# Kernel optimization log

Hardware: AMD Instinct MI355X
Metric: run time of the kernel (lower is better)

## Reference

```python
import jax, jax.numpy as jnp
import numpy as np
import math

N_HEAD = 16

def _c(a):
    # stack real/imag -> complex64
    return jax.lax.complex(a[..., 0], a[..., 1])

def _rope_phasor(T, D, dtype=jnp.float32):
    inv_freq = 1.0 / (10000.0 ** (jnp.arange(D, dtype=dtype) / D))
    t = jnp.arange(T, dtype=dtype)
    freqs = jnp.outer(t, inv_freq)  # [T, D]
    return jax.lax.complex(jnp.cos(freqs), jnp.sin(freqs))

def setup_inputs() -> dict:
    key = jax.random.key(0)
    ks = jax.random.split(key, 9)
    B, T, C = 2, 1024, 1024
    s = 0.02
    return {
        "x":  jax.random.normal(ks[0], (B, T, C, 2), jnp.float32),
        "wq": jax.random.normal(ks[1], (C, C, 2), jnp.float32) * s,
        "bq": jax.random.normal(ks[2], (C, 2), jnp.float32) * s,
        "wk": jax.random.normal(ks[3], (C, C, 2), jnp.float32) * s,
        "bk": jax.random.normal(ks[4], (C, 2), jnp.float32) * s,
        "wv": jax.random.normal(ks[5], (C, C, 2), jnp.float32) * s,
        "bv": jax.random.normal(ks[6], (C, 2), jnp.float32) * s,
        "wo": jax.random.normal(ks[7], (C, C, 2), jnp.float32) * s,
        "bo": jax.random.normal(ks[8], (C, 2), jnp.float32) * s,
    }

def reference(x, wq, bq, wk, bk, wv, bv, wo, bo):
    B, T, C, _ = x.shape
    H = N_HEAD
    D = C // H
    xc = _c(x)
    # complex linear projections: y = x @ W^T + b
    q = xc @ _c(wq).T + _c(bq)
    k = xc @ _c(wk).T + _c(bk)
    v = xc @ _c(wv).T + _c(bv)
    # [B, T, C] -> [B, H, T, D]
    q = q.reshape(B, T, H, D).transpose(0, 2, 1, 3)
    k = k.reshape(B, T, H, D).transpose(0, 2, 1, 3)
    v = v.reshape(B, T, H, D).transpose(0, 2, 1, 3)
    # complex RoPE phasor multiply
    ph = _rope_phasor(T, D)[None, None]  # [1,1,T,D]
    q = q * ph
    k = k * ph
    # complex QK^H, scaled
    score = jnp.einsum('bhtd,bhsd->bhts', q, jnp.conj(k)) / math.sqrt(D)
    # softmax over magnitude, then real-valued complex weights
    attn = jax.nn.softmax(jnp.abs(score), axis=-1)
    attn_c = jax.lax.complex(attn, jnp.zeros_like(attn))
    out = jnp.einsum('bhts,bhsd->bhtd', attn_c, v)
    out = out.transpose(0, 2, 1, 3).reshape(B, T, C)
    out = out @ _c(wo).T + _c(bo)
    # return real/imag stacked for a real-valued harness
    return jnp.stack([out.real, out.imag], axis=-1)
```

## Files before the change

### kernel.cpp

```cpp
#include <hip/hip_runtime.h>
#include <math.h>

#define T_SEQ  1024
#define C_DIM  1024
#define NH_    16
#define H_DIM  64
#define SCL    (0.125f * 1.4426950408889634f)

typedef __bf16 bf16;
typedef __bf16 bf16x4 __attribute__((ext_vector_type(4)));
typedef __bf16 bf16x8 __attribute__((ext_vector_type(8)));
typedef float  f32x4  __attribute__((ext_vector_type(4)));

#define MFMA16(a, b, c) __builtin_amdgcn_mfma_f32_16x16x32_bf16(a, b, c, 0, 0, 0)

#define GLOAD_LDS16(g, l) __builtin_amdgcn_global_load_lds( \
    (const __attribute__((address_space(1))) void*)(g),     \
    (__attribute__((address_space(3))) void*)(l), 16, 0, 0)

__device__ __forceinline__ bf16x8 neg8(bf16x8 x) {
    union { bf16x8 v; unsigned int u[4]; } t;
    t.v = x;
    t.u[0] ^= 0x80008000u; t.u[1] ^= 0x80008000u;
    t.u[2] ^= 0x80008000u; t.u[3] ^= 0x80008000u;
    return t.v;
}

__device__ __forceinline__ bf16x8 frag_sw(const bf16* plane, int row, int chunk) {
    int c = chunk ^ (row & 7);
    return *(const bf16x8*)&plane[row * 64 + c * 8];
}
__device__ __forceinline__ bf16x8 frag_sw4b(const bf16* plane, int row, int chunk) {
    int c = chunk ^ ((row >> 1) & 3);
    return *(const bf16x8*)&plane[row * 32 + c * 8];
}

__global__ __launch_bounds__(256)
void split_all(const float* __restrict__ x,  const float* __restrict__ wq,
               const float* __restrict__ wk, const float* __restrict__ wv,
               const float* __restrict__ wo,
               bf16* Xr, bf16* Xi, bf16* Wqr, bf16* Wqi, bf16* Wkr, bf16* Wki,
               bf16* Wvr, bf16* Wvi, bf16* Wor, bf16* Woi,
               float* __restrict__ rope)
{
    int z = blockIdx.y;
    if (z == 5) {
        if (blockIdx.x >= 256) return;
        int idx = blockIdx.x * 256 + threadIdx.x;
        int tp = idx >> 6, d = idx & 63;
        float invf = exp2f((float)d * -0.2076205059304601f);
        float fr = (float)tp * invf;
        float sn, cs; sincosf(fr, &sn, &cs);
        *(float2*)&rope[(size_t)idx * 2] = make_float2(cs, sn);
        return;
    }
    if (z > 0 && blockIdx.x >= 512) return;
    const float* in; bf16 *pr, *pi;
    if      (z == 0) { in = x;  pr = Xr;  pi = Xi;  }
    else if (z == 1) { in = wq; pr = Wqr; pi = Wqi; }
    else if (z == 2) { in = wk; pr = Wkr; pi = Wki; }
    else if (z == 3) { in = wv; pr = Wvr; pi = Wvi; }
    else             { in = wo; pr = Wor; pi = Woi; }
    int idx = (blockIdx.x * 256 + threadIdx.x) * 8;
    bf16x8 r, im;
#pragma unroll
    for (int j = 0; j < 4; j++) {
        float4 v = *(const float4*)(in + (size_t)idx * 2 + j * 4);
        r[2*j]   = (bf16)v.x; im[2*j]   = (bf16)v.y;
        r[2*j+1] = (bf16)v.z; im[2*j+1] = (bf16)v.w;
    }
    *(bf16x8*)(pr + idx) = r;
    *(bf16x8*)(pi + idx) = im;
}

__global__ __launch_bounds__(512, 2)
void qkv_gemm(const bf16* __restrict__ Xr, const bf16* __restrict__ Xi,
              const bf16* __restrict__ Wqr, const bf16* __restrict__ Wqi,
              const bf16* __restrict__ Wkr, const bf16* __restrict__ Wki,
              const bf16* __restrict__ Wvr, const bf16* __restrict__ Wvi,
              const float* __restrict__ bq, const float* __restrict__ bk,
              const float* __restrict__ bv, const float* __restrict__ rope,
              bf16* Qr, bf16* Qi, bf16* Kr, bf16* Ki, bf16* Vr, bf16* Vi)
{
    __shared__ __attribute__((aligned(16))) bf16 smem[40960];
    const int t = threadIdx.x, lane = t & 63, wave = t >> 6;
    const int wm = (wave >> 1) * 32, wn = (wave & 1) * 32;
    const int lm = lane & 15, quad = lane >> 4;
    const int lr4 = lane >> 2, sc4 = ((lane & 3) ^ ((lane >> 3) & 3)) * 8;
    const int h = blockIdx.x, m0 = blockIdx.y * 128, n0 = h * 64;

    auto stage = [&](int k0, int bsel) {
        bf16* bb_ = smem + bsel * 20480;
#pragma unroll
        for (int j = 0; j < 5; j++) {
            int c = wave + 8 * j;
            const bf16* src; bf16* dst;
            if (c < 8)       {                 src = Xr  + (size_t)(m0 + c * 16 + lr4) * C_DIM + k0 + sc4; dst = bb_ + c * 512; }
            else if (c < 16) { int u = c - 8;  src = Xi  + (size_t)(m0 + u * 16 + lr4) * C_DIM + k0 + sc4; dst = bb_ + 4096  + u * 512; }
            else if (c < 20) { int u = c - 16; src = Wqr + (size_t)(n0 + u * 16 + lr4) * C_DIM + k0 + sc4; dst = bb_ + 8192  + u * 512; }
            else if (c < 24) { int u = c - 20; src = Wqi + (size_t)(n0 + u * 16 + lr4) * C_DIM + k0 + sc4; dst = bb_ + 10240 + u * 512; }
            else if (c < 28) { int u = c - 24; src = Wkr + (size_t)(n0 + u * 16 + lr4) * C_DIM + k0 + sc4; dst = bb_ + 12288 + u * 512; }
            else if (c < 32) { int u = c - 28; src = Wki + (size_t)(n0 + u * 16 + lr4) * C_DIM + k0 + sc4; dst = bb_ + 14336 + u * 512; }
            else if (c < 36) { int u = c - 32; src = Wvr + (size_t)(n0 + u * 16 + lr4) * C_DIM + k0 + sc4; dst = bb_ + 16384 + u * 512; }
            else             { int u = c - 36; src = Wvi + (size_t)(n0 + u * 16 + lr4) * C_DIM + k0 + sc4; dst = bb_ + 18432 + u * 512; }
            GLOAD_LDS16(src, dst);
        }
    };

    f32x4 accr[3][2][2], acci[3][2][2];
#pragma unroll
    for (int p = 0; p < 3; p++)
#pragma unroll
        for (int i = 0; i < 2; i++)
#pragma unroll
            for (int j = 0; j < 2; j++) { accr[p][i][j] = (f32x4)0.f; acci[p][i][j] = (f32x4)0.f; }

    stage(0, 0);
    for (int it = 0; it < 32; it++) {
        __syncthreads();
        if (it < 31) stage((it + 1) * 32, (it + 1) & 1);
        const bf16* buf = smem + (it & 1) * 20480;

        bf16x8 ar[2], ai_[2];
#pragma unroll
        for (int i = 0; i < 2; i++) {
            ar[i]  = frag_sw4b(buf,        wm + i * 16 + lm, quad);
            ai_[i] = frag_sw4b(buf + 4096, wm + i * 16 + lm, quad);
        }
#pragma unroll
        for (int p = 0; p < 3; p++) {
            const bf16* bp = buf + 8192 + p * 4096;
            bf16x8 br_[2], bi_[2], bn_[2];
#pragma unroll
            for (int j = 0; j < 2; j++) {
                br_[j] = frag_sw4b(bp,        wn + j * 16 + lm, quad);
                bi_[j] = frag_sw4b(bp + 2048, wn + j * 16 + lm, quad);
                bn_[j] = neg8(bi_[j]);
            }
#pragma unroll
            for (int i = 0; i < 2; i++)
#pragma unroll
                for (int j = 0; j < 2; j++) {
                    accr[p][i][j] = MFMA16(ar[i],  br_[j], accr[p][i][j]);
                    accr[p][i][j] = MFMA16(ai_[i], bn_[j], accr[p][i][j]);
                    acci[p][i][j] = MFMA16(ar[i],  bi_[j], acci[p][i][j]);
                    acci[p][i][j] = MFMA16(ai_[i], br_[j], acci[p][i][j]);
                }
        }
    }

    const int bb = m0 >> 10, tbase = m0 & (T_SEQ - 1);

#pragma unroll
    for (int p = 0; p < 2; p++) {
        const float* bias = p ? bk : bq;
#pragma unroll
        for (int i = 0; i < 2; i++)
#pragma unroll
            for (int j = 0; j < 2; j++) {
                int d = wn + j * 16 + lm;
                float2 bv = *(const float2*)&bias[2 * (n0 + d)];
#pragma unroll
                for (int r = 0; r < 4; r++) {
                    int tpos = tbase + wm + i * 16 + quad * 4 + r;
                    float2 ph = *(const float2*)&rope[((size_t)tpos * H_DIM + d) * 2];
                    float yr = accr[p][i][j][r] + bv.x;
                    float yi = acci[p][i][j][r] + bv.y;
                    accr[p][i][j][r] = yr * ph.x - yi * ph.y;
                    acci[p][i][j][r] = yr * ph.y + yi * ph.x;
                }
            }
        bf16* dr = (p ? Kr : Qr) + ((size_t)(bb * NH_ + h) * T_SEQ + tbase) * H_DIM;
        bf16* di = (p ? Ki : Qi) + ((size_t)(bb * NH_ + h) * T_SEQ + tbase) * H_DIM;
#pragma unroll
        for (int pass = 0; pass < 2; pass++) {
            __syncthreads();
#pragma unroll
            for (int i = 0; i < 2; i++)
#pragma unroll
                for (int j = 0; j < 2; j++)
#pragma unroll
                    for (int r = 0; r < 4; r++)
                        smem[(wm + i * 16 + quad * 4 + r) * 72 + wn + j * 16 + lm] =
                            (bf16)(pass ? acci[p][i][j][r] : accr[p][i][j][r]);
            __syncthreads();
            bf16* dst = pass ? di : dr;
#pragma unroll
            for (int pp = 0; pp < 2; pp++) {
                int ch = t + 512 * pp;
                int row = ch >> 3, o = (ch & 7) * 8;
                *(bf16x8*)&dst[row * H_DIM + o] = *(const bf16x8*)&smem[row * 72 + o];
            }
        }
    }

    {
        bf16* dsts[2] = { Vr, Vi };
#pragma unroll
        for (int pass = 0; pass < 2; pass++) {
            __syncthreads();
#pragma unroll
            for (int i = 0; i < 2; i++)
#pragma unroll
                for (int j = 0; j < 2; j++) {
                    int d = wn + j * 16 + lm;
                    float2 bv = *(const float2*)&bv[0], bvv = *(const float2*)&bv;
                }
            break;
        }
    }
    {
#pragma unroll
        for (int pass = 0; pass < 2; pass++) {
            __syncthreads();
#pragma unroll
            for (int i = 0; i < 2; i++)
#pragma unroll
                for (int j = 0; j < 2; j++) {
                    int d = wn + j * 16 + lm;
                    float2 bvv = *(const float2*)&bv[2 * (n0 + d)];
                    float bb2 = pass ? bvv.y : bvv.x;
                    bf16x4 pk;
#pragma unroll
                    for (int r = 0; r < 4; r++)
                        pk[r] = (bf16)((pass ? acci[2][i][j][r] : accr[2][i][j][r]) + bb2);
                    *(bf16x4*)&smem[d * 136 + wm + i * 16 + quad * 4] = pk;
                }
            __syncthreads();
            bf16* dst = (pass ? Vi : Vr) + ((size_t)(bb * NH_ + h) * H_DIM) * T_SEQ + tbase;
#pragma unroll
            for (int pp = 0; pp < 2; pp++) {
                int ch = t + 512 * pp;
                int row = ch >> 4, o = (ch & 15) * 8;
                *(bf16x8*)&dst[(size_t)row * T_SEQ + o] = *(const bf16x8*)&smem[row * 136 + o];
            }
        }
    }
}

__global__ __launch_bounds__(256, 4)
void out_gemm(const bf16* __restrict__ Ar, const bf16* __restrict__ Ai,
              const bf16* __restrict__ Br, const bf16* __restrict__ Bi,
              const float* __restrict__ bias, float* __restrict__ Y)
{
    __shared__ __attribute__((aligned(16))) bf16 sm[16384];
    const int t = threadIdx.x, lane = t & 63, wave = t >> 6;
    const int lm = lane & 15, quad = lane >> 4;
    const int s_lr = lane >> 3, s_c = (lane & 7) ^ s_lr;
    const int wm = (wave >> 1) * 32, wn = (wave & 1) * 32;
    const int m0 = blockIdx.y * 64, n0 = blockIdx.x * 64;

    f32x4 accr[2][2], acci[2][2];
#pragma unroll
    for (int i = 0; i < 2; i++)
#pragma unroll
        for (int j = 0; j < 2; j++) { accr[i][j] = (f32x4)0.f; acci[i][j] = (f32x4)0.f; }

    for (int k0 = 0; k0 < C_DIM; k0 += 64) {
#pragma unroll
        for (int j = 0; j < 8; j++) {
            int c = wave + 4 * j;
            const bf16* src; bf16* dst;
            if (c < 8)       {             src = Ar + (size_t)(m0 + c * 8 + s_lr) * C_DIM + k0 + s_c * 8; dst = sm + c * 512; }
            else if (c < 16) { int u = c - 8;  src = Ai + (size_t)(m0 + u * 8 + s_lr) * C_DIM + k0 + s_c * 8; dst = sm + 4096 + u * 512; }
            else if (c < 24) { int u = c - 16; src = Br + (size_t)(n0 + u * 8 + s_lr) * C_DIM + k0 + s_c * 8; dst = sm + 8192 + u * 512; }
            else             { int u = c - 24; src = Bi + (size_t)(n0 + u * 8 + s_lr) * C_DIM + k0 + s_c * 8; dst = sm + 12288 + u * 512; }
            GLOAD_LDS16(src, dst);
        }
        __syncthreads();
#pragma unroll
        for (int kh = 0; kh < 2; kh++) {
            bf16x8 ar[2], ai_[2], br_[2], bi_[2], bn_[2];
#pragma unroll
            for (int i = 0; i < 2; i++) {
                ar[i]  = frag_sw(sm,        wm + i * 16 + lm, kh * 4 + quad);
                ai_[i] = frag_sw(sm + 4096, wm + i * 16 + lm, kh * 4 + quad);
            }
#pragma unroll
            for (int j = 0; j < 2; j++) {
                br_[j] = frag_sw(sm + 8192,  wn + j * 16 + lm, kh * 4 + quad);
                bi_[j] = frag_sw(sm + 12288, wn + j * 16 + lm, kh * 4 + quad);
                bn_[j] = neg8(bi_[j]);
            }
#pragma unroll
            for (int i = 0; i < 2; i++)
#pragma unroll
                for (int j = 0; j < 2; j++) {
                    accr[i][j] = MFMA16(ar[i],  br_[j], accr[i][j]);
                    accr[i][j] = MFMA16(ai_[i], bn_[j], accr[i][j]);
                    acci[i][j] = MFMA16(ar[i],  bi_[j], acci[i][j]);
                    acci[i][j] = MFMA16(ai_[i], br_[j], acci[i][j]);
                }
        }
        __syncthreads();
    }
#pragma unroll
    for (int i = 0; i < 2; i++)
#pragma unroll
        for (int j = 0; j < 2; j++) {
            int n = n0 + wn + j * 16 + lm;
            float2 bvv = *(const float2*)&bias[2 * n];
#pragma unroll
            for (int r = 0; r < 4; r++) {
                int m = m0 + wm + i * 16 + quad * 4 + r;
                *(float2*)&Y[((size_t)m * C_DIM + n) * 2] =
                    make_float2(accr[i][j][r] + bvv.x, acci[i][j][r] + bvv.y);
            }
        }
}

__global__ __launch_bounds__(512, 4)
void attn_mfma(const bf16* __restrict__ Qpr, const bf16* __restrict__ Qpi,
               const bf16* __restrict__ Kpr, const bf16* __restrict__ Kpi,
               const bf16* __restrict__ Vtr, const bf16* __restrict__ Vti,
               bf16* __restrict__ ABr, bf16* __restrict__ ABi)
{
    __shared__ __attribute__((aligned(16))) bf16 smem[32768];
    const int t = threadIdx.x, lane = t & 63, w = t >> 6;
    const int qg = w & 3, sh = w >> 2;
    const int lm = lane & 15, quad = lane >> 4;
    const int q0 = blockIdx.x * 64;
    const int h = blockIdx.y, b = blockIdx.z;
    const size_t hb = (size_t)(b * NH_ + h) * T_SEQ * H_DIM;
    const int s_lr = lane >> 3, s_c = (lane & 7) ^ s_lr;
    const int lr4 = lane >> 2, sc4 = ((lane & 3) ^ ((lane >> 3) & 3)) * 8;

    {
        const bf16* gq = (sh ? Qpi : Qpr) + hb + (size_t)q0 * H_DIM;
        bf16* lq = smem + 16384 + sh * 4096;
#pragma unroll
        for (int j = 0; j < 2; j++) {
            int cc = qg * 2 + j;
            GLOAD_LDS16(gq + (cc * 8 + s_lr) * H_DIM + s_c * 8, lq + cc * 512);
        }
    }
    __syncthreads();

    bf16x8 qfr[2], qfi[2], nqfr[2];
#pragma unroll
    for (int kh = 0; kh < 2; kh++) {
        qfr[kh]  = frag_sw(smem + 16384, qg * 16 + lm, kh * 4 + quad);
        qfi[kh]  = frag_sw(smem + 20480, qg * 16 + lm, kh * 4 + quad);
        nqfr[kh] = neg8(qfr[kh]);
    }

#pragma unroll
    for (int pre = 0; pre < 1; pre++) {
        const int S = sh * 512;
        bf16* bd = smem + sh * 8192;
        if (qg < 2) {
            const bf16* g = (qg ? Kpi : Kpr) + hb + (size_t)S * H_DIM;
            bf16* d = bd + (qg ? 2048 : 0);
#pragma unroll
            for (int cc = 0; cc < 4; cc++)
                GLOAD_LDS16(g + (cc * 8 + s_lr) * H_DIM + s_c * 8, d + cc * 512);
        } else {
            const bf16* g = (qg == 2 ? Vtr : Vti) + hb + S;
            bf16* d = bd + (qg == 2 ? 4096 : 6144);
#pragma unroll
            for (int cc = 0; cc < 4; cc++)
                GLOAD_LDS16(g + (size_t)(cc * 16 + lr4) * T_SEQ + sc4, d + cc * 512);
        }
    }

    f32x4 Or[4], Oi[4];
#pragma unroll
    for (int nt = 0; nt < 4; nt++) { Or[nt] = (f32x4)0.f; Oi[nt] = (f32x4)0.f; }
    float lsum = 0.f;
    const int idxA = (((2 * quad) & 3) * 16 + lm) * 4;
    const int idxB = idxA + 64;
    const bool hisel = quad >= 2;

    for (int it = 0; it < 16; it++) {
        __syncthreads();
        if (it < 15) {
            const int S = (it + 1) * 32 + sh * 512;
            bf16* bd = smem + ((it + 1) & 1) * 16384 + sh * 8192;
            if (qg < 2) {
                const bf16* g = (qg ? Kpi : Kpr) + hb + (size_t)S * H_DIM;
                bf16* d = bd + (qg ? 2048 : 0);
#pragma unroll
                for (int cc = 0; cc < 4; cc++)
                    GLOAD_LDS16(g + (cc * 8 + s_lr) * H_DIM + s_c * 8, d + cc * 512);
            } else {
                const bf16* g = (qg == 2 ? Vtr : Vti) + hb + S;
                bf16* d = bd + (qg == 2 ? 4096 : 6144);
#pragma unroll
                for (int cc = 0; cc < 4; cc++)
                    GLOAD_LDS16(g + (size_t)(cc * 16 + lr4) * T_SEQ + sc4, d + cc * 512);
            }
        }
        const bf16* buf = smem + (it & 1) * 16384 + sh * 8192;

        union { unsigned int u[2]; bf16 b[4]; } pk[2];
        float lsA = 0.f, lsB = 0.f;
#pragma unroll
        for (int ct = 0; ct < 2; ct++) {
            f32x4 sre = (f32x4)0.f, sim = (f32x4)0.f;
            __builtin_amdgcn_s_setprio(1);
#pragma unroll
            for (int kh = 0; kh < 2; kh++) {
                bf16x8 kr = frag_sw(buf,        ct * 16 + lm, kh * 4 + quad);
                bf16x8 ki = frag_sw(buf + 2048, ct * 16 + lm, kh * 4 + quad);
                sre = MFMA16(kr, qfr[kh],  sre);
                sre = MFMA16(ki, qfi[kh],  sre);
                sim = MFMA16(kr, qfi[kh],  sim);
                sim = MFMA16(ki, nqfr[kh], sim);
            }
            __builtin_amdgcn_s_setprio(0);
#pragma unroll
            for (int r = 0; r < 4; r++) {
                float mag2 = fmaf(sre[r], sre[r], sim[r] * sim[r]);
                float p = __builtin_amdgcn_exp2f(__builtin_amdgcn_sqrtf(mag2) * SCL);
                if (ct) lsB += p; else lsA += p;
                pk[ct].b[r] = (bf16)p;
            }
        }
        lsum += lsA + lsB;

        union { unsigned int u[4]; bf16x8 v; } pf;
        {
            int a0 = __builtin_amdgcn_ds_bpermute(idxA, (int)pk[0].u[0]);
            int a1 = __builtin_amdgcn_ds_bpermute(idxA, (int)pk[1].u[0]);
            int b0 = __builtin_amdgcn_ds_bpermute(idxA, (int)pk[0].u[1]);
            int b1 = __builtin_amdgcn_ds_bpermute(idxA, (int)pk[1].u[1]);
            int c0 = __builtin_amdgcn_ds_bpermute(idxB, (int)pk[0].u[0]);
            int c1 = __builtin_amdgcn_ds_bpermute(idxB, (int)pk[1].u[0]);
            int d0 = __builtin_amdgcn_ds_bpermute(idxB, (int)pk[0].u[1]);
            int d1 = __builtin_amdgcn_ds_bpermute(idxB, (int)pk[1].u[1]);
            pf.u[0] = (unsigned int)(hisel ? a1 : a0);
            pf.u[1] = (unsigned int)(hisel ? b1 : b0);
            pf.u[2] = (unsigned int)(hisel ? c1 : c0);
            pf.u[3] = (unsigned int)(hisel ? d1 : d0);
        }

        __builtin_amdgcn_s_setprio(1);
#pragma unroll
        for (int nt = 0; nt < 4; nt++) {
            Or[nt] = MFMA16(pf.v, frag_sw4b(buf + 4096, nt * 16 + lm, quad), Or[nt]);
            Oi[nt] = MFMA16(pf.v, frag_sw4b(buf + 6144, nt * 16 + lm, quad), Oi[nt]);
        }
        __builtin_amdgcn_s_setprio(0);
    }

    lsum += __shfl_xor(lsum, 16);
    lsum += __shfl_xor(lsum, 32);

    __syncthreads();
    float* Of  = (float*)smem;
    float* lsc = Of + 128 * 66;
    if (sh == 1) {
#pragma unroll
        for (int nt = 0; nt < 4; nt++)
#pragma unroll
            for (int r = 0; r < 4; r++) {
                Of[((qg * 2 + 0) * 16 + quad * 4 + r) * 66 + nt * 16 + lm] = Or[nt][r];
                Of[((qg * 2 + 1) * 16 + quad * 4 + r) * 66 + nt * 16 + lm] = Oi[nt][r];
            }
        if (quad == 0) lsc[qg * 16 + lm] = lsum;
    }
    __syncthreads();
    if (sh == 0) {
        float ltot = lsum + lsc[qg * 16 + lm];
        float lv = 1.f / ltot;
        float linv[4];
#pragma unroll
        for (int r = 0; r < 4; r++)
            linv[r] = __shfl(lv, (quad << 4) + quad * 4 + r, 64);
        size_t mbase = (size_t)(b * T_SEQ + q0 + qg * 16 + quad * 4) * C_DIM;
        int colb = h * H_DIM + lm;
#pragma unroll
        for (int nt = 0; nt < 4; nt++)
#pragma unroll
            for (int r = 0; r < 4; r++) {
                float orv = Or[nt][r] + Of[((qg * 2 + 0) * 16 + quad * 4 + r) * 66 + nt * 16 + lm];
                float oiv = Oi[nt][r] + Of[((qg * 2 + 1) * 16 + quad * 4 + r) * 66 + nt * 16 + lm];
                size_t o = mbase + (size_t)r * C_DIM + colb + nt * 16;
                ABr[o] = (bf16)(orv * linv[r]);
                ABi[o] = (bf16)(oiv * linv[r]);
            }
    }
}

extern "C" void kernel_launch(void* const* d_in, const int* in_sizes, int n_in,
                              void* d_out, int out_size, void* d_ws, size_t ws_size,
                              hipStream_t stream) {
    const float* x  = (const float*)d_in[0];
    const float* wq = (const float*)d_in[1];
    const float* bq = (const float*)d_in[2];
    const float* wk = (const float*)d_in[3];
    const float* bk = (const float*)d_in[4];
    const float* wv = (const float*)d_in[5];
    const float* bv = (const float*)d_in[6];
    const float* wo = (const float*)d_in[7];
    const float* bo = (const float*)d_in[8];

    float* rope = (float*)d_ws;
    bf16* w = (bf16*)(rope + 131072);
    const size_t MSZ = (size_t)2048 * 1024;
    const size_t WSZ = (size_t)1024 * 1024;
    const size_t PSZ = (size_t)2 * NH_ * T_SEQ * H_DIM;

    bf16 *Xr = w, *Xi = Xr + MSZ;
    bf16 *Wqr = Xi + MSZ,  *Wqi = Wqr + WSZ;
    bf16 *Wkr = Wqi + WSZ, *Wki = Wkr + WSZ;
    bf16 *Wvr = Wki + WSZ, *Wvi = Wvr + WSZ;
    bf16 *Wor = Wvi + WSZ, *Woi = Wor + WSZ;
    bf16 *Qr = Woi + WSZ, *Qi = Qr + PSZ;
    bf16 *Kr = Qi + PSZ,  *Ki = Kr + PSZ;
    bf16 *Vr = Ki + PSZ,  *Vi = Vr + PSZ;
    bf16 *ABr = Vi + PSZ, *ABi = ABr + MSZ;

    split_all<<<dim3(1024, 6), 256, 0, stream>>>(x, wq, wk, wv, wo,
        Xr, Xi, Wqr, Wqi, Wkr, Wki, Wvr, Wvi, Wor, Woi, rope);

    qkv_gemm<<<dim3(16, 16), 512, 0, stream>>>(
        Xr, Xi, Wqr, Wqi, Wkr, Wki, Wvr, Wvi, bq, bk, bv, rope,
        Qr, Qi, Kr, Ki, Vr, Vi);

    attn_mfma<<<dim3(16, 16, 2), 512, 0, stream>>>(
        Qr, Qi, Kr, Ki, Vr, Vi, ABr, ABi);

    out_gemm<<<dim3(16, 32), 256, 0, stream>>>(ABr, ABi, Wor, Woi, bo, (float*)d_out);
}
```

Before: 213.9 us.

## Triple-buffer QKV GEMM with interleaved staging and manual waitcnt scheduling

The QKV projection GEMM moves from double to triple buffering in LDS. Global-to-LDS loads for tile k+2 are split into chunks issued between the Q, K and V MFMA phases, and vmcnt waits with raw s_barrier replace __syncthreads, so memory latency overlaps compute with finer-grained sync. The attention kernel's V-tile swizzle changes from a row>>1-based XOR to a row&3 XOR, on both the global-to-LDS write and the fragment read, to alter LDS bank patterns. Costs are 50% more LDS per block, which may lower occupancy, and a fragile hand-counted vmcnt that must match the number of loads in flight.

```diff
diff --git a/kernel.cpp b/kernel.cpp
--- a/kernel.cpp
+++ b/kernel.cpp
@@ -11,6 +11,8 @@
 typedef __bf16 bf16x4 __attribute__((ext_vector_type(4)));
 typedef __bf16 bf16x8 __attribute__((ext_vector_type(8)));
 typedef float  f32x4  __attribute__((ext_vector_type(4)));
+
+template<bool B> struct BC { static constexpr bool value = B; };
 
 #define MFMA16(a, b, c) __builtin_amdgcn_mfma_f32_16x16x32_bf16(a, b, c, 0, 0, 0)
 
@@ -29,6 +31,10 @@
 __device__ __forceinline__ bf16x8 frag_sw(const bf16* plane, int row, int chunk) {
     int c = chunk ^ (row & 7);
     return *(const bf16x8*)&plane[row * 64 + c * 8];
+}
+__device__ __forceinline__ bf16x8 frag_sw4(const bf16* plane, int row, int chunk) {
+    int c = chunk ^ (row & 3);
+    return *(const bf16x8*)&plane[row * 32 + c * 8];
 }
 __device__ __forceinline__ bf16x8 frag_sw4b(const bf16* plane, int row, int chunk) {
     int c = chunk ^ ((row >> 1) & 3);
@@ -82,29 +88,25 @@
               const float* __restrict__ bv, const float* __restrict__ rope,
               bf16* Qr, bf16* Qi, bf16* Kr, bf16* Ki, bf16* Vr, bf16* Vi)
 {
-    __shared__ __attribute__((aligned(16))) bf16 smem[40960];
+    __shared__ __attribute__((aligned(16))) bf16 smem[61440];
     const int t = threadIdx.x, lane = t & 63, wave = t >> 6;
     const int wm = (wave >> 1) * 32, wn = (wave & 1) * 32;
     const int lm = lane & 15, quad = lane >> 4;
-    const int lr4 = lane >> 2, sc4 = ((lane & 3) ^ ((lane >> 3) & 3)) * 8;
+    const int lr4 = lane >> 2, sc4q = ((lane & 3) ^ ((lane >> 3) & 3)) * 8;
     const int h = blockIdx.x, m0 = blockIdx.y * 128, n0 = h * 64;
 
-    auto stage = [&](int k0, int bsel) {
-        bf16* bb_ = smem + bsel * 20480;
-#pragma unroll
-        for (int j = 0; j < 5; j++) {
-            int c = wave + 8 * j;
-            const bf16* src; bf16* dst;
-            if (c < 8)       {                 src = Xr  + (size_t)(m0 + c * 16 + lr4) * C_DIM + k0 + sc4; dst = bb_ + c * 512; }
-            else if (c < 16) { int u = c - 8;  src = Xi  + (size_t)(m0 + u * 16 + lr4) * C_DIM + k0 + sc4; dst = bb_ + 4096  + u * 512; }
-            else if (c < 20) { int u = c - 16; src = Wqr + (size_t)(n0 + u * 16 + lr4) * C_DIM + k0 + sc4; dst = bb_ + 8192  + u * 512; }
-            else if (c < 24) { int u = c - 20; src = Wqi + (size_t)(n0 + u * 16 + lr4) * C_DIM + k0 + sc4; dst = bb_ + 10240 + u * 512; }
-            else if (c < 28) { int u = c - 24; src = Wkr + (size_t)(n0 + u * 16 + lr4) * C_DIM + k0 + sc4; dst = bb_ + 12288 + u * 512; }
-            else if (c < 32) { int u = c - 28; src = Wki + (size_t)(n0 + u * 16 + lr4) * C_DIM + k0 + sc4; dst = bb_ + 14336 + u * 512; }
-            else if (c < 36) { int u = c - 32; src = Wvr + (size_t)(n0 + u * 16 + lr4) * C_DIM + k0 + sc4; dst = bb_ + 16384 + u * 512; }
-            else             { int u = c - 36; src = Wvi + (size_t)(n0 + u * 16 + lr4) * C_DIM + k0 + sc4; dst = bb_ + 18432 + u * 512; }
-            GLOAD_LDS16(src, dst);
-        }
+    auto stage1 = [&](bf16* bb_, int j, int k0) {
+        int c = wave + 8 * j;
+        const bf16* src; bf16* dst;
+        if (c < 8)       {                 src = Xr  + (size_t)(m0 + c * 16 + lr4) * C_DIM + k0 + sc4q; dst = bb_ + c * 512; }
+        else if (c < 16) { int u = c - 8;  src = Xi  + (size_t)(m0 + u * 16 + lr4) * C_DIM + k0 + sc4q; dst = bb_ + 4096  + u * 512; }
+        else if (c < 20) { int u = c - 16; src = Wqr + (size_t)(n0 + u * 16 + lr4) * C_DIM + k0 + sc4q; dst = bb_ + 8192  + u * 512; }
+        else if (c < 24) { int u = c - 20; src = Wqi + (size_t)(n0 + u * 16 + lr4) * C_DIM + k0 + sc4q; dst = bb_ + 10240 + u * 512; }
+        else if (c < 28) { int u = c - 24; src = Wkr + (size_t)(n0 + u * 16 + lr4) * C_DIM + k0 + sc4q; dst = bb_ + 12288 + u * 512; }
+        else if (c < 32) { int u = c - 28; src = Wki + (size_t)(n0 + u * 16 + lr4) * C_DIM + k0 + sc4q; dst = bb_ + 14336 + u * 512; }
+        else if (c < 36) { int u = c - 32; src = Wvr + (size_t)(n0 + u * 16 + lr4) * C_DIM + k0 + sc4q; dst = bb_ + 16384 + u * 512; }
+        else             { int u = c - 36; src = Wvi + (size_t)(n0 + u * 16 + lr4) * C_DIM + k0 + sc4q; dst = bb_ + 18432 + u * 512; }
+        GLOAD_LDS16(src, dst);
     };
 
     f32x4 accr[3][2][2], acci[3][2][2];
@@ -115,39 +117,99 @@
 #pragma unroll
             for (int j = 0; j < 2; j++) { accr[p][i][j] = (f32x4)0.f; acci[p][i][j] = (f32x4)0.f; }
 
-    stage(0, 0);
-    for (int it = 0; it < 32; it++) {
-        __syncthreads();
-        if (it < 31) stage((it + 1) * 32, (it + 1) & 1);
-        const bf16* buf = smem + (it & 1) * 20480;
-
-        bf16x8 ar[2], ai_[2];
+    auto step = [&](auto DOSTAGE, auto DRAIN, int bufsel, int sbsel, int k2) {
+        const bf16* buf = smem + bufsel * 20480;
+        bf16* sb = smem + sbsel * 20480;
+        if constexpr (DRAIN.value)
+            asm volatile("s_waitcnt vmcnt(0)\n\ts_barrier" ::: "memory");
+        else
+            asm volatile("s_waitcnt vmcnt(5)\n\ts_barrier" ::: "memory");
+
+        bf16x8 ar[2], ai_[2], br_[2], bi_[2], bn_[2];
 #pragma unroll
         for (int i = 0; i < 2; i++) {
             ar[i]  = frag_sw4b(buf,        wm + i * 16 + lm, quad);
             ai_[i] = frag_sw4b(buf + 4096, wm + i * 16 + lm, quad);
         }
 #pragma unroll
-        for (int p = 0; p < 3; p++) {
-            const bf16* bp = buf + 8192 + p * 4096;
-            bf16x8 br_[2], bi_[2], bn_[2];
+        for (int j = 0; j < 2; j++) {
+            br_[j] = frag_sw4b(buf + 8192,  wn + j * 16 + lm, quad);
+            bi_[j] = frag_sw4b(buf + 10240, wn + j * 16 + lm, quad);
+        }
+        if constexpr (DOSTAGE.value) { stage1(sb, 0, k2); stage1(sb, 1, k2); }
+        asm volatile("s_waitcnt lgkmcnt(0)" ::: "memory");
+        __builtin_amdgcn_sched_barrier(0);
+        __builtin_amdgcn_s_setprio(1);
+#pragma unroll
+        for (int j = 0; j < 2; j++) bn_[j] = neg8(bi_[j]);
+#pragma unroll
+        for (int i = 0; i < 2; i++)
 #pragma unroll
             for (int j = 0; j < 2; j++) {
-                br_[j] = frag_sw4b(bp,        wn + j * 16 + lm, quad);
-                bi_[j] = frag_sw4b(bp + 2048, wn + j * 16 + lm, quad);
-                bn_[j] = neg8(bi_[j]);
-            }
-#pragma unroll
-            for (int i = 0; i < 2; i++)
-#pragma unroll
-                for (int j = 0; j < 2; j++) {
-                    accr[p][i][j] = MFMA16(ar[i],  br_[j], accr[p][i][j]);
-                    accr[p][i][j] = MFMA16(ai_[i], bn_[j], accr[p][i][j]);
-                    acci[p][i][j] = MFMA16(ar[i],  bi_[j], acci[p][i][j]);
-                    acci[p][i][j] = MFMA16(ai_[i], br_[j], acci[p][i][j]);
-                }
-        }
-    }
+                accr[0][i][j] = MFMA16(ar[i],  br_[j], accr[0][i][j]);
+                accr[0][i][j] = MFMA16(ai_[i], bn_[j], accr[0][i][j]);
+                acci[0][i][j] = MFMA16(ar[i],  bi_[j], acci[0][i][j]);
+                acci[0][i][j] = MFMA16(ai_[i], br_[j], acci[0][i][j]);
+            }
+        __builtin_amdgcn_s_setprio(0);
+        __builtin_amdgcn_s_barrier();
+#pragma unroll
+        for (int j = 0; j < 2; j++) {
+            br_[j] = frag_sw4b(buf + 12288, wn + j * 16 + lm, quad);
+            bi_[j] = frag_sw4b(buf + 14336, wn + j * 16 + lm, quad);
+        }
+        if constexpr (DOSTAGE.value) { stage1(sb, 2, k2); stage1(sb, 3, k2); }
+        asm volatile("s_waitcnt lgkmcnt(0)" ::: "memory");
+        __builtin_amdgcn_sched_barrier(0);
+        __builtin_amdgcn_s_setprio(1);
+#pragma unroll
+        for (int j = 0; j < 2; j++) bn_[j] = neg8(bi_[j]);
+#pragma unroll
+        for (int i = 0; i < 2; i++)
+#pragma unroll
+            for (int j = 0; j < 2; j++) {
+                accr[1][i][j] = MFMA16(ar[i],  br_[j], accr[1][i][j]);
+                accr[1][i][j] = MFMA16(ai_[i], bn_[j], accr[1][i][j]);
+                acci[1][i][j] = MFMA16(ar[i],  bi_[j], acci[1][i][j]);
+                acci[1][i][j] = MFMA16(ai_[i], br_[j], acci[1][i][j]);
+            }
+        __builtin_amdgcn_s_setprio(0);
+        __builtin_amdgcn_s_barrier();
+#pragma unroll
+        for (int j = 0; j < 2; j++) {
+            br_[j] = frag_sw4b(buf + 16384, wn + j * 16 + lm, quad);
+            bi_[j] = frag_sw4b(buf + 18432, wn + j * 16 + lm, quad);
+        }
+        if constexpr (DOSTAGE.value) { stage1(sb, 4, k2); }
+        asm volatile("s_waitcnt lgkmcnt(0)" ::: "memory");
+        __builtin_amdgcn_sched_barrier(0);
+        __builtin_amdgcn_s_setprio(1);
+#pragma unroll
+        for (int j = 0; j < 2; j++) bn_[j] = neg8(bi_[j]);
+#pragma unroll
+        for (int i = 0; i < 2; i++)
+#pragma unroll
+            for (int j = 0; j < 2; j++) {
+                accr[2][i][j] = MFMA16(ar[i],  br_[j], accr[2][i][j]);
+                accr[2][i][j] = MFMA16(ai_[i], bn_[j], accr[2][i][j]);
+                acci[2][i][j] = MFMA16(ar[i],  bi_[j], acci[2][i][j]);
+                acci[2][i][j] = MFMA16(ai_[i], br_[j], acci[2][i][j]);
+            }
+        __builtin_amdgcn_s_setprio(0);
+    };
+
+#pragma unroll
+    for (int j = 0; j < 5; j++) stage1(smem,         j, 0);
+#pragma unroll
+    for (int j = 0; j < 5; j++) stage1(smem + 20480, j, 32);
+
+    for (int base = 0; base < 30; base += 3) {
+        step(BC<true>{}, BC<false>{}, 0, 2, (base + 2) * 32);
+        step(BC<true>{}, BC<false>{}, 1, 0, (base + 3) * 32);
+        step(BC<true>{}, BC<false>{}, 2, 1, (base + 4) * 32);
+    }
+    step(BC<false>{}, BC<false>{}, 0, 0, 0);
+    step(BC<false>{}, BC<true >{}, 1, 0, 0);
 
     const int bb = m0 >> 10, tbase = m0 & (T_SEQ - 1);
 
@@ -159,13 +221,13 @@
 #pragma unroll
             for (int j = 0; j < 2; j++) {
                 int d = wn + j * 16 + lm;
-                float2 bv = *(const float2*)&bias[2 * (n0 + d)];
+                float2 bvv = *(const float2*)&bias[2 * (n0 + d)];
 #pragma unroll
                 for (int r = 0; r < 4; r++) {
                     int tpos = tbase + wm + i * 16 + quad * 4 + r;
                     float2 ph = *(const float2*)&rope[((size_t)tpos * H_DIM + d) * 2];
-                    float yr = accr[p][i][j][r] + bv.x;
-                    float yi = acci[p][i][j][r] + bv.y;
+                    float yr = accr[p][i][j][r] + bvv.x;
+                    float yi = acci[p][i][j][r] + bvv.y;
                     accr[p][i][j][r] = yr * ph.x - yi * ph.y;
                     acci[p][i][j][r] = yr * ph.y + yi * ph.x;
                 }
@@ -194,21 +256,6 @@
         }
     }
 
-    {
-        bf16* dsts[2] = { Vr, Vi };
-#pragma unroll
-        for (int pass = 0; pass < 2; pass++) {
-            __syncthreads();
-#pragma unroll
-            for (int i = 0; i < 2; i++)
-#pragma unroll
-                for (int j = 0; j < 2; j++) {
-                    int d = wn + j * 16 + lm;
-                    float2 bv = *(const float2*)&bv[0], bvv = *(const float2*)&bv;
-                }
-            break;
-        }
-    }
     {
 #pragma unroll
         for (int pass = 0; pass < 2; pass++) {
@@ -323,7 +370,7 @@
     const int h = blockIdx.y, b = blockIdx.z;
     const size_t hb = (size_t)(b * NH_ + h) * T_SEQ * H_DIM;
     const int s_lr = lane >> 3, s_c = (lane & 7) ^ s_lr;
-    const int lr4 = lane >> 2, sc4 = ((lane & 3) ^ ((lane >> 3) & 3)) * 8;
+    const int lr4 = lane >> 2, sc4a = ((lane & 3) ^ (lr4 & 3)) * 8;
 
     {
         const bf16* gq = (sh ? Qpi : Qpr) + hb + (size_t)q0 * H_DIM;
@@ -359,7 +406,7 @@
             bf16* d = bd + (qg == 2 ? 4096 : 6144);
 #pragma unroll
             for (int cc = 0; cc < 4; cc++)
-                GLOAD_LDS16(g + (size_t)(cc * 16 + lr4) * T_SEQ + sc4, d + cc * 512);
+                GLOAD_LDS16(g + (size_t)(cc * 16 + lr4) * T_SEQ + sc4a, d + cc * 512);
         }
     }
 
@@ -387,7 +434,7 @@
                 bf16* d = bd + (qg == 2 ? 4096 : 6144);
 #pragma unroll
                 for (int cc = 0; cc < 4; cc++)
-                    GLOAD_LDS16(g + (size_t)(cc * 16 + lr4) * T_SEQ + sc4, d + cc * 512);
+                    GLOAD_LDS16(g + (size_t)(cc * 16 + lr4) * T_SEQ + sc4a, d + cc * 512);
             }
         }
         const bf16* buf = smem + (it & 1) * 16384 + sh * 8192;
@@ -437,8 +484,8 @@
         __builtin_amdgcn_s_setprio(1);
 #pragma unroll
         for (int nt = 0; nt < 4; nt++) {
-            Or[nt] = MFMA16(pf.v, frag_sw4b(buf + 4096, nt * 16 + lm, quad), Or[nt]);
-            Oi[nt] = MFMA16(pf.v, frag_sw4b(buf + 6144, nt * 16 + lm, quad), Oi[nt]);
+            Or[nt] = MFMA16(pf.v, frag_sw4(buf + 4096, nt * 16 + lm, quad), Or[nt]);
+            Oi[nt] = MFMA16(pf.v, frag_sw4(buf + 6144, nt * 16 + lm, quad), Oi[nt]);
         }
         __builtin_amdgcn_s_setprio(0);
     }
```

Measured after the change: 210.4 us. Within noise of the previous version (-1.6%).
